# Kernel optimization log

Hardware: AMD Instinct MI355X
Metric: run time of the kernel (lower is better)

Reference implementation:

```python
import jax, jax.numpy as jnp
import numpy as np

COST_CLASS = 1.0
COST_L1 = 1.0


def _lsa(cost):
    """Exact rectangular linear sum assignment (Jonker-Volgenant / e-maxx Hungarian).
    cost: (n, m) numpy float64 with n <= m. Returns ans[n]: column assigned to each row.
    """
    n, m = cost.shape
    INF = np.inf
    u = np.zeros(n + 1)
    v = np.zeros(m + 1)
    p = np.zeros(m + 1, dtype=np.int64)    # p[j]: 1-indexed row matched to column j (0 = free)
    way = np.zeros(m + 1, dtype=np.int64)
    for i in range(1, n + 1):
        p[0] = i
        j0 = 0
        minv = np.full(m + 1, INF)
        used = np.zeros(m + 1, dtype=bool)
        while True:
            used[j0] = True
            i0 = p[j0]
            minv1 = minv[1:]               # view, in-place updates propagate
            jmask = ~used[1:]
            cur = cost[i0 - 1, :] - u[i0] - v[1:]
            upd = jmask & (cur < minv1)
            minv1[upd] = cur[upd]
            way[1:][upd] = j0
            idx = np.nonzero(jmask)[0]
            j1rel = idx[np.argmin(minv1[idx])]
            delta = minv1[j1rel]
            u[p[used]] += delta
            v[used] -= delta
            minv1[jmask] -= delta
            j0 = j1rel + 1
            if p[j0] == 0:
                break
        # augment along the alternating path
        while j0:
            j1 = way[j0]
            p[j0] = p[j1]
            j0 = j1
    ans = np.zeros(n, dtype=np.int64)
    for j in range(1, m + 1):
        if p[j] > 0:
            ans[p[j] - 1] = j - 1
    return ans


def _solve_blocks(blocks):
    """blocks: (B, Q, T) numpy. Per-batch optimal assignment, scipy-compatible output:
    row_ind sorted ascending, min(Q,T) pairs (here Q >= T so T pairs)."""
    blocks = np.asarray(blocks, dtype=np.float64)
    B, Q, T = blocks.shape
    rows = np.empty((B, T), dtype=np.int32)
    cols = np.empty((B, T), dtype=np.int32)
    for b in range(B):
        c = blocks[b]
        if Q >= T:
            ans = _lsa(c.T)                      # ans[t] = matched query q
            order = np.argsort(ans, kind="stable")
            rows[b] = ans[order]
            cols[b] = order
        else:
            ans = _lsa(c)
            rows[b] = np.arange(Q)
            cols[b] = ans
    return rows, cols


def _cost_blocks(outputs, targets):
    """Diagonal (per-sample) blocks of the DETR cost matrix.
    outputs: (B, Q, 1+P); targets: (B, T, 1+P). Returns (B, Q, T).
    Math identical to building the full (B*Q, B*T) matrix and slicing, as in the source."""
    out_prob = jax.nn.softmax(outputs[:, :, 0], axis=-1)      # softmax over the QUERY axis (as in source)
    out_pos = outputs[:, :, 1:]                                # (B, Q, P)
    tgt_pos = targets[:, :, 1:]                                # (B, T, P)
    cost_l1 = jnp.abs(out_pos[:, :, None, :] - tgt_pos[:, None, :, :]).sum(-1)  # L1 cdist, (B, Q, T)
    return COST_CLASS * (-out_prob[:, :, None]) + COST_L1 * cost_l1


def setup_inputs() -> dict:
    key = jax.random.key(0)
    k1, k2 = jax.random.split(key)
    outputs = jax.random.normal(k1, (8, 2048, 3), dtype=jnp.float32)
    targets = jax.random.uniform(k2, (8, 256, 3), dtype=jnp.float32)
    return {"outputs": outputs, "targets": targets}


def reference(outputs, targets):
    blocks = _cost_blocks(outputs, targets)                    # (B, Q, T)
    B, Q, T = blocks.shape
    n = min(Q, T)
    shapes = (jax.ShapeDtypeStruct((B, n), jnp.int32),
              jax.ShapeDtypeStruct((B, n), jnp.int32))
    row_ind, col_ind = jax.pure_callback(_solve_blocks, shapes, blocks)
    return row_ind, col_ind
```

## Files before the change

### kernel.cpp

```cpp
#include <hip/hip_runtime.h>


constexpr int B = 8;
constexpr int Q = 2048;
constexpr int T = 256;
constexpr int NT = 256;
constexpr int KPT = Q / NT;
constexpr int NW = NT / 64;
constexpr double DINF = 1e300;

struct __align__(16) CD { double u; float tx, ty; };

__device__ __forceinline__ unsigned wave_min_u32_dpp(unsigned a) {
  int v = (int)a, t;
  t = __builtin_amdgcn_update_dpp(v, v, 0x111, 0xf, 0xf, false);
  v = ((unsigned)t < (unsigned)v) ? t : v;
  t = __builtin_amdgcn_update_dpp(v, v, 0x112, 0xf, 0xf, false);
  v = ((unsigned)t < (unsigned)v) ? t : v;
  t = __builtin_amdgcn_update_dpp(v, v, 0x114, 0xf, 0xf, false);
  v = ((unsigned)t < (unsigned)v) ? t : v;
  t = __builtin_amdgcn_update_dpp(v, v, 0x118, 0xf, 0xf, false);
  v = ((unsigned)t < (unsigned)v) ? t : v;
  t = __builtin_amdgcn_update_dpp(v, v, 0x142, 0xf, 0xf, false);
  v = ((unsigned)t < (unsigned)v) ? t : v;
  t = __builtin_amdgcn_update_dpp(v, v, 0x143, 0xf, 0xf, false);
  v = ((unsigned)t < (unsigned)v) ? t : v;
  return (unsigned)__builtin_amdgcn_readlane(v, 63);
}

__launch_bounds__(NT, 1)
__global__ void hungarian_dpp(const float* __restrict__ outs,
                              const float* __restrict__ tgts,
                              int* __restrict__ out) {
  const int b = blockIdx.x;
  const int tid = threadIdx.x;
  const int lane = tid & 63;
  const int wv = tid >> 6;

  __shared__ CD colDat[Q + 1];
  __shared__ CD rowDat[T + 1];
  __shared__ short p[Q + 1];
  __shared__ short visCol[T + 8];
  __shared__ double visD[T + 8];
  __shared__ unsigned phi[2][NW], plo[2][NW];
  __shared__ int pix[2][NW];
  __shared__ int ansArr[T];
  __shared__ double s_rv[NW];
  __shared__ float sh_f;

  const size_t qbase = (size_t)b * Q;
  const size_t tbase = (size_t)b * T;

  float xs[KPT], qx[KPT], qy[KPT];
#pragma unroll
  for (int k = 0; k < KPT; ++k) {
    const size_t o = (qbase + tid + k * NT) * 3;
    xs[k] = outs[o];
    qx[k] = outs[o + 1];
    qy[k] = outs[o + 2];
  }
  {
    const size_t o = (tbase + tid) * 3;
    rowDat[tid + 1].tx = tgts[o + 1];
    rowDat[tid + 1].ty = tgts[o + 2];
    rowDat[tid + 1].u = 0.0;
    if (tid == 0) { rowDat[0].tx = 0.f; rowDat[0].ty = 0.f; rowDat[0].u = 0.0; }
  }

  float lmax = xs[0];
#pragma unroll
  for (int k = 1; k < KPT; ++k) lmax = fmaxf(lmax, xs[k]);
  for (int off = 32; off > 0; off >>= 1) lmax = fmaxf(lmax, __shfl_down(lmax, off));
  if ((tid & 63) == 0) s_rv[tid >> 6] = (double)lmax;
  __syncthreads();
  if (tid == 0) {
    float m2 = (float)s_rv[0];
    for (int w = 1; w < NW; ++w) m2 = fmaxf(m2, (float)s_rv[w]);
    sh_f = m2;
  }
  __syncthreads();
  const float smax = sh_f;
  float ex[KPT];
  float lsum = 0.f;
#pragma unroll
  for (int k = 0; k < KPT; ++k) { ex[k] = expf(xs[k] - smax); lsum += ex[k]; }
  for (int off = 32; off > 0; off >>= 1) lsum += __shfl_down(lsum, off);
  if ((tid & 63) == 0) s_rv[tid >> 6] = (double)lsum;
  __syncthreads();
  if (tid == 0) {
    float s2 = 0.f;
    for (int w = 0; w < NW; ++w) s2 += (float)s_rv[w];
    sh_f = s2;
  }
  __syncthreads();
  const float ssum = sh_f;
  float np_[KPT];
#pragma unroll
  for (int k = 0; k < KPT; ++k) np_[k] = -(ex[k] / ssum);

  for (int j = tid; j <= Q; j += NT) p[j] = 0;
  if (tid == 0) visCol[0] = 0;
  double vreg[KPT];
#pragma unroll
  for (int k = 0; k < KPT; ++k) vreg[k] = 0.0;
  __syncthreads();

  for (int i = 1; i <= T; ++i) {
    if (tid == 0) p[0] = (short)i;
    unsigned usedMask = 0;
    double D = 0.0;
    __syncthreads();
    double ui0 = rowDat[i].u;
    float tX = rowDat[i].tx, tY = rowDat[i].ty;
    int s = 0, S;

    for (;;) {
      double bval = DINF;
      int bidx = 0x7fffffff;
#pragma unroll
      for (int k = 0; k < KPT; ++k) {
        const float cf = fabsf(qx[k] - tX) + fabsf(qy[k] - tY) + np_[k];
        double cur = ((double)cf - ui0) - vreg[k];
        if (usedMask & (1u << k)) cur = DINF;
        if (cur < bval) { bval = cur; bidx = 1 + tid + (k << 8); }
      }
      bval += 0.0;
      const long long bb = __double_as_longlong(bval);
      const unsigned long long key = (unsigned long long)bb ^
          ((bb < 0) ? 0xFFFFFFFFFFFFFFFFull : 0x8000000000000000ull);
      const unsigned khi = (unsigned)(key >> 32);
      const unsigned klo = (unsigned)key;

      const unsigned minhi = wave_min_u32_dpp(khi);
      const unsigned long long mask = __ballot(khi == minhi);
      unsigned wklo; int widx;
      if (__popcll(mask) == 1) {
        const int wl = (int)__ffsll(mask) - 1;
        wklo = (unsigned)__builtin_amdgcn_readlane((int)klo, wl);
        widx = __builtin_amdgcn_readlane(bidx, wl);
      } else {
        wklo = 0xffffffffu; widx = 0x7fffffff;
        unsigned long long mm = mask;
        while (mm) {
          const int l = (int)__ffsll(mm) - 1; mm &= mm - 1;
          const unsigned lo2 = (unsigned)__builtin_amdgcn_readlane((int)klo, l);
          const int ix2 = __builtin_amdgcn_readlane(bidx, l);
          if (lo2 < wklo || (lo2 == wklo && ix2 < widx)) { wklo = lo2; widx = ix2; }
        }
      }
      const int par = s & 1;
      if (lane == 0) { phi[par][wv] = minhi; plo[par][wv] = wklo; pix[par][wv] = widx; }
      if (tid == 0) visD[s] = D;
      __syncthreads();

      unsigned long long bk = ((unsigned long long)phi[par][0] << 32) | plo[par][0];
      int bj = pix[par][0];
#pragma unroll
      for (int w = 1; w < NW; ++w) {
        const unsigned long long k2 =
            ((unsigned long long)phi[par][w] << 32) | plo[par][w];
        const int j2 = pix[par][w];
        if (k2 < bk || (k2 == bk && j2 < bj)) { bk = k2; bj = j2; }
      }
      const long long db = (long long)((bk & 0x8000000000000000ull)
                                           ? (bk ^ 0x8000000000000000ull) : ~bk);
      D += __longlong_as_double(db);
      const int j1 = bj;
      if (tid == ((j1 - 1) & 255)) usedMask |= 1u << ((j1 - 1) >> 8);
      if (tid == 0) visCol[s + 1] = (short)j1;
      const int pj1 = (int)p[j1];
      const CD cd = colDat[j1];
      ++s;
      if (pj1 == 0) { S = s; break; }
      ui0 = cd.u; tX = cd.tx; tY = cd.ty;
    }

    __syncthreads();
    const double Dfin = D;
    const int rr0 = (tid < S) ? (int)p[(int)visCol[tid]] : 0;
    __syncthreads();
    if (tid < S) {
      const int cnew = (int)visCol[tid + 1];
      p[cnew] = (short)rr0;
      const double unew = rowDat[rr0].u + (Dfin - visD[tid]);
      rowDat[rr0].u = unew;
      CD cd2; cd2.u = unew; cd2.tx = rowDat[rr0].tx; cd2.ty = rowDat[rr0].ty;
      colDat[cnew] = cd2;
    }
    for (int sv = 1; sv < S; ++sv) {
      const int qv = (int)visCol[sv] - 1;
      if ((qv & 255) == tid) vreg[qv >> 8] -= (Dfin - visD[sv]);
    }
  }
  __syncthreads();

  for (int j = 1 + tid; j <= Q; j += NT) {
    const int pi = (int)p[j];
    if (pi > 0) ansArr[pi - 1] = j - 1;
  }
  __syncthreads();
  const int a = ansArr[tid];
  int rank = 0;
  for (int t2 = 0; t2 < T; ++t2) rank += (ansArr[t2] < a) ? 1 : 0;
  out[(size_t)b * T + rank] = a;
  out[(size_t)B * T + (size_t)b * T + rank] = tid;
}

extern "C" void kernel_launch(void* const* d_in, const int* in_sizes, int n_in,
                              void* d_out, int out_size, void* d_ws, size_t ws_size,
                              hipStream_t stream) {
  const float* outs = (const float*)d_in[0];
  const float* tgts = (const float*)d_in[1];
  int* out = (int*)d_out;
  hungarian_dpp<<<B, NT, 0, stream>>>(outs, tgts, out);
}
```

Before: 1.027 ms.

## Replace per-step block barrier with generation-tagged LDS polling in Hungarian loop

Each Dijkstra step in the inner search loop used to end at a __syncthreads so that the per-wave minima could be combined. Now each wave publishes its minimum key and index into double-buffered 64-bit LDS slots tagged with a generation counter. Every wave spin-polls until all slots carry the current tag, which removes the workgroup barrier from the critical path of every step. The per-thread argmin over the 8 columns also becomes a pairwise tree instead of a serial chain. The cost is busy-wait LDS traffic and reliance on relaxed-ordering visibility. The 20-bit tag can also wrap on very long runs.

```diff
diff --git a/kernel.cpp b/kernel.cpp
--- a/kernel.cpp
+++ b/kernel.cpp
@@ -29,9 +29,9 @@
 }
 
 __launch_bounds__(NT, 1)
-__global__ void hungarian_dpp(const float* __restrict__ outs,
-                              const float* __restrict__ tgts,
-                              int* __restrict__ out) {
+__global__ void hungarian_poll(const float* __restrict__ outs,
+                               const float* __restrict__ tgts,
+                               int* __restrict__ out) {
   const int b = blockIdx.x;
   const int tid = threadIdx.x;
   const int lane = tid & 63;
@@ -42,8 +42,8 @@
   __shared__ short p[Q + 1];
   __shared__ short visCol[T + 8];
   __shared__ double visD[T + 8];
-  __shared__ unsigned phi[2][NW], plo[2][NW];
-  __shared__ int pix[2][NW];
+  alignas(8) __shared__ unsigned long long slotA[2][NW];
+  alignas(8) __shared__ unsigned long long slotB[2][NW];
   __shared__ int ansArr[T];
   __shared__ double s_rv[NW];
   __shared__ float sh_f;
@@ -66,6 +66,10 @@
     rowDat[tid + 1].u = 0.0;
     if (tid == 0) { rowDat[0].tx = 0.f; rowDat[0].ty = 0.f; rowDat[0].u = 0.0; }
   }
+  if (tid < 2 * NW) {
+    ((unsigned long long*)slotA)[tid] = 0ull;
+    ((unsigned long long*)slotB)[tid] = 0ull;
+  }
 
   float lmax = xs[0];
 #pragma unroll
@@ -103,6 +107,7 @@
   double vreg[KPT];
 #pragma unroll
   for (int k = 0; k < KPT; ++k) vreg[k] = 0.0;
+  unsigned g = 1;
   __syncthreads();
 
   for (int i = 1; i <= T; ++i) {
@@ -115,15 +120,28 @@
     int s = 0, S;
 
     for (;;) {
-      double bval = DINF;
-      int bidx = 0x7fffffff;
+      double cv[KPT];
 #pragma unroll
       for (int k = 0; k < KPT; ++k) {
         const float cf = fabsf(qx[k] - tX) + fabsf(qy[k] - tY) + np_[k];
         double cur = ((double)cf - ui0) - vreg[k];
         if (usedMask & (1u << k)) cur = DINF;
-        if (cur < bval) { bval = cur; bidx = 1 + tid + (k << 8); }
-      }
+        cv[k] = cur;
+      }
+      double v0 = cv[0]; int k0 = 0;
+      if (cv[1] < v0) { v0 = cv[1]; k0 = 1; }
+      double v1 = cv[2]; int k1 = 2;
+      if (cv[3] < v1) { v1 = cv[3]; k1 = 3; }
+      double v2 = cv[4]; int k2 = 4;
+      if (cv[5] < v2) { v2 = cv[5]; k2 = 5; }
+      double v3 = cv[6]; int k3 = 6;
+      if (cv[7] < v3) { v3 = cv[7]; k3 = 7; }
+      if (v1 < v0) { v0 = v1; k0 = k1; }
+      if (v3 < v2) { v2 = v3; k2 = k3; }
+      double bval = v0; int bk = k0;
+      if (v2 < v0) { bval = v2; bk = k2; }
+      int bidx = 1 + tid + (bk << 8);
+
       bval += 0.0;
       const long long bb = __double_as_longlong(bval);
       const unsigned long long key = (unsigned long long)bb ^
@@ -148,22 +166,42 @@
           if (lo2 < wklo || (lo2 == wklo && ix2 < widx)) { wklo = lo2; widx = ix2; }
         }
       }
+
       const int par = s & 1;
-      if (lane == 0) { phi[par][wv] = minhi; plo[par][wv] = wklo; pix[par][wv] = widx; }
+      const unsigned gs = g & 0xFFFFFu;
+      if (lane == 0) {
+        const unsigned long long Bwr = ((unsigned long long)wklo << 32) | gs;
+        const unsigned long long Awr = ((unsigned long long)minhi << 32) |
+            ((unsigned long long)((unsigned)widx & 0xFFFu) << 20) | gs;
+        __atomic_store_n(&slotB[par][wv], Bwr, __ATOMIC_RELAXED);
+        __atomic_store_n(&slotA[par][wv], Awr, __ATOMIC_RELAXED);
+      }
       if (tid == 0) visD[s] = D;
-      __syncthreads();
-
-      unsigned long long bk = ((unsigned long long)phi[par][0] << 32) | plo[par][0];
-      int bj = pix[par][0];
+
+      unsigned long long Aw[NW], Bw[NW];
+      for (;;) {
+        bool all = true;
+#pragma unroll
+        for (int w = 0; w < NW; ++w) {
+          Aw[w] = __atomic_load_n(&slotA[par][w], __ATOMIC_RELAXED);
+          Bw[w] = __atomic_load_n(&slotB[par][w], __ATOMIC_RELAXED);
+          all = all && ((unsigned)(Aw[w] & 0xFFFFFu) == gs)
+                    && ((unsigned)(Bw[w] & 0xFFFFFu) == gs);
+        }
+        if (all) break;
+      }
+      ++g;
+
+      unsigned long long bkk = ((Aw[0] >> 32) << 32) | (Bw[0] >> 32);
+      int bj = (int)((Aw[0] >> 20) & 0xFFFu);
 #pragma unroll
       for (int w = 1; w < NW; ++w) {
-        const unsigned long long k2 =
-            ((unsigned long long)phi[par][w] << 32) | plo[par][w];
-        const int j2 = pix[par][w];
-        if (k2 < bk || (k2 == bk && j2 < bj)) { bk = k2; bj = j2; }
-      }
-      const long long db = (long long)((bk & 0x8000000000000000ull)
-                                           ? (bk ^ 0x8000000000000000ull) : ~bk);
+        const unsigned long long k2b = ((Aw[w] >> 32) << 32) | (Bw[w] >> 32);
+        const int j2 = (int)((Aw[w] >> 20) & 0xFFFu);
+        if (k2b < bkk || (k2b == bkk && j2 < bj)) { bkk = k2b; bj = j2; }
+      }
+      const long long db = (long long)((bkk & 0x8000000000000000ull)
+                                           ? (bkk ^ 0x8000000000000000ull) : ~bkk);
       D += __longlong_as_double(db);
       const int j1 = bj;
       if (tid == ((j1 - 1) & 255)) usedMask |= 1u << ((j1 - 1) >> 8);
@@ -212,5 +250,5 @@
   const float* outs = (const float*)d_in[0];
   const float* tgts = (const float*)d_in[1];
   int* out = (int*)d_out;
-  hungarian_dpp<<<B, NT, 0, stream>>>(outs, tgts, out);
+  hungarian_poll<<<B, NT, 0, stream>>>(outs, tgts, out);
 }
```

Result: slower. 1.090 ms (+6.1%).
